# Kernel optimization log

Measured on AMD Instinct MI355X. Metric: run time of the kernel, lower is better.

The kernel has to match this reference:

```python
import jax, jax.numpy as jnp
import numpy as np

B, T, E, H, G = 8, 1024, 1024, 16, 4
D = E // H
SCALING = D ** -0.5
READER_W = 0.1  # reader_group_weight


def _heads(x):
    # [B, T, E] -> [B, H, T, D]
    return x.reshape(B, T, H, D).transpose(0, 2, 1, 3)


def setup_inputs() -> dict:
    key = jax.random.key(0)
    ks = jax.random.split(key, 16)
    s = 0.02
    return {
        "hidden_states": jax.random.normal(ks[0], (B, T, E), jnp.float32),
        "reader_token": jax.random.randint(ks[1], (B,), 0, G, dtype=jnp.int32),
        # shared (generic) projections, torch Linear convention: y = x @ W.T + b
        "Wq": jax.random.normal(ks[2], (E, E), jnp.float32) * s,
        "bq": jnp.zeros((E,), jnp.float32),
        "Wk": jax.random.normal(ks[3], (E, E), jnp.float32) * s,
        "bk": jnp.zeros((E,), jnp.float32),
        "Wv": jax.random.normal(ks[4], (E, E), jnp.float32) * s,
        "bv": jnp.zeros((E,), jnp.float32),
        "Wo": jax.random.normal(ks[5], (E, E), jnp.float32) * s,
        "bo": jnp.zeros((E,), jnp.float32),
        # stacked per-reader-group expert projections [G, E, E]
        "RWq": jax.random.normal(ks[6], (G, E, E), jnp.float32) * s,
        "Rbq": jnp.zeros((G, E), jnp.float32),
        "RWk": jax.random.normal(ks[7], (G, E, E), jnp.float32) * s,
        "Rbk": jnp.zeros((G, E), jnp.float32),
        "RWv": jax.random.normal(ks[8], (G, E, E), jnp.float32) * s,
        "Rbv": jnp.zeros((G, E), jnp.float32),
    }


def reference(hidden_states, reader_token, Wq, bq, Wk, bk, Wv, bv, Wo, bo,
              RWq, Rbq, RWk, Rbk, RWv, Rbv):
    hs = hidden_states
    # --- generic attention probs (shared weights) ---
    q = _heads((hs @ Wq.T + bq) * SCALING)          # [B,H,T,D]
    k = _heads(hs @ Wk.T + bk)                       # [B,H,T,D]
    v = _heads(hs @ Wv.T + bv)                       # [B,H,T,D]
    gen_probs = jax.nn.softmax(jnp.einsum('bhtd,bhsd->bhts', q, k), axis=-1)
    # --- reader-group attention probs (per-sample routed weights) ---
    Wq_b = RWq[reader_token]                          # [B,E,E]
    Wk_b = RWk[reader_token]
    q_r = _heads((jnp.einsum('bte,boe->bto', hs, Wq_b) + Rbq[reader_token][:, None, :]) * SCALING)
    k_r = _heads(jnp.einsum('bte,boe->bto', hs, Wk_b) + Rbk[reader_token][:, None, :])
    rdr_probs = jax.nn.softmax(jnp.einsum('bhtd,bhsd->bhts', q_r, k_r), axis=-1)
    # --- weighted combine, then attend over GENERIC value states ---
    probs = (READER_W * rdr_probs + (1.0 - READER_W) * gen_probs) / 2.0
    attn = jnp.einsum('bhts,bhsd->bhtd', probs, v)    # [B,H,T,D]
    attn = attn.transpose(0, 2, 1, 3).reshape(B, T, E)
    return attn @ Wo.T + bo
```

## Files before the change

kernel.cpp:

```cpp
#include <hip/hip_runtime.h>
#include <stdint.h>

#define AS1 __attribute__((address_space(1)))
#define AS3 __attribute__((address_space(3)))

typedef __attribute__((ext_vector_type(8))) short bf16x8;
typedef __attribute__((ext_vector_type(4))) float f32x4;

#define NB 8
#define NT 1024
#define NE 1024
#define NH 16
#define BT (NB * NT)

__device__ __forceinline__ unsigned short f2bf(float f) {
    unsigned int u = __builtin_bit_cast(unsigned int, f);
    u += 0x7FFFu + ((u >> 16) & 1u);
    return (unsigned short)(u >> 16);
}
__device__ __forceinline__ unsigned short f2bfu(float f) {
    unsigned int u = __builtin_bit_cast(unsigned int, f);
    return (unsigned short)((u + 0x8000u) >> 16);
}

__global__ void k_cvt(const float* __restrict__ in, unsigned short* __restrict__ out, int n) {
    int i = (blockIdx.x * 256 + threadIdx.x) * 4;
    if (i >= n) return;
    float4 f = *reinterpret_cast<const float4*>(in + i);
    ushort4 o;
    o.x = f2bf(f.x); o.y = f2bf(f.y); o.z = f2bf(f.z); o.w = f2bf(f.w);
    *reinterpret_cast<ushort4*>(out + i) = o;
}

struct GJob {
    const unsigned short* W;
    const float* bias;
    void* out;
    float scale;
    int routed;
};

template <bool OUT_F32>
__global__ __launch_bounds__(512, 2)
void k_gemm256(const unsigned short* __restrict__ A,
               GJob j0, GJob j1, GJob j2, GJob j3, GJob j4,
               const int* __restrict__ rt, int cpx)
{
    __shared__ __attribute__((aligned(16))) unsigned short LB[2][2][2][128 * 64];

    const int flat = blockIdx.x;
    const int wgid = (flat & 7) * cpx + (flat >> 3);
    const int pz  = wgid >> 7;
    const int rem = wgid & 127;
    const int by = rem >> 2, bx = rem & 3;
    const int m0 = by << 8, n0 = bx << 8;

    GJob jb = j0;
    if (pz == 1) jb = j1;
    else if (pz == 2) jb = j2;
    else if (pz == 3) jb = j3;
    else if (pz == 4) jb = j4;
    int g = jb.routed ? rt[m0 >> 10] : 0;
    const unsigned short* Wg = jb.W + (size_t)g * NE * NE;

    const int tid  = threadIdx.x;
    const int wid  = tid >> 6;
    const int lane = tid & 63;
    const int frow = lane & 15;
    const int g4   = lane >> 4;
    const int wm = wid >> 2, wn = wid & 3;

    const int rh0  = tid >> 3;
    const int swz8 = ((tid & 7) ^ (rh0 & 7)) * 8;
    const unsigned short* baseA = A  + (size_t)m0 * NE;
    const unsigned short* baseB = Wg + (size_t)n0 * NE;

    auto STAGE = [&](int d, int mat, int half, int kt) {
        const unsigned short* base = mat ? baseB : baseA;
#pragma unroll
        for (int j = 0; j < 2; ++j) {
            const unsigned short* src =
                base + (size_t)(half * 128 + rh0 + j * 64) * NE + kt * 64 + swz8;
            __builtin_amdgcn_global_load_lds((AS1 void*)src,
                (AS3 void*)&LB[d][mat][half][(wid * 64 + j * 512) * 8], 16, 0, 0);
        }
    };

    f32x4 acc[8][4];
#pragma unroll
    for (int m = 0; m < 8; ++m)
#pragma unroll
        for (int n = 0; n < 4; ++n) acc[m][n] = (f32x4){0.f, 0.f, 0.f, 0.f};

    bf16x8 a4[4], b4[4];
    auto RDA = [&](int d, int mh, int kh) {
#pragma unroll
        for (int mf = 0; mf < 4; ++mf) {
            int rh = mh * 64 + mf * 16 + frow;
            int off = rh * 64 + (((kh * 4 + g4) ^ (frow & 7)) * 8);
            a4[mf] = *reinterpret_cast<const bf16x8*>(&LB[d][0][wm][off]);
        }
    };
    auto RDB = [&](int d, int kh) {
#pragma unroll
        for (int nf = 0; nf < 4; ++nf) {
            int rh = (wn & 1) * 64 + nf * 16 + frow;
            int off = rh * 64 + (((kh * 4 + g4) ^ (frow & 7)) * 8);
            b4[nf] = *reinterpret_cast<const bf16x8*>(&LB[d][1][wn >> 1][off]);
        }
    };
    auto MM = [&](int mh) {
        __builtin_amdgcn_s_setprio(1);
#pragma unroll
        for (int mf = 0; mf < 4; ++mf)
#pragma unroll
            for (int nf = 0; nf < 4; ++nf)
                acc[mh * 4 + mf][nf] =
                    __builtin_amdgcn_mfma_f32_16x16x32_bf16(a4[mf], b4[nf], acc[mh * 4 + mf][nf], 0, 0, 0);
        __builtin_amdgcn_s_setprio(0);
    };

#define BARX __builtin_amdgcn_s_barrier()
#define LGK0 asm volatile("s_waitcnt lgkmcnt(0)" ::: "memory")
#define VMC2 asm volatile("s_waitcnt vmcnt(2)" ::: "memory")

    STAGE(0, 0, 0, 0); STAGE(0, 0, 1, 0); STAGE(0, 1, 0, 0); STAGE(0, 1, 1, 0);
    STAGE(1, 1, 0, 1);
    VMC2; BARX;

#pragma unroll 1
    for (int i = 0; i < 8; ++i) {
        const int t = 2 * i;
        const bool pre = (i < 7);
        RDA(0, 0, 0); RDB(0, 0); STAGE(1, 1, 1, t + 1);
        BARX; LGK0; MM(0); BARX;
        RDA(0, 1, 0); STAGE(1, 0, 0, t + 1);
        BARX; LGK0; MM(1); BARX;
        RDA(0, 0, 1); RDB(0, 1); STAGE(1, 0, 1, t + 1);
        BARX; LGK0; MM(0); BARX;
        RDA(0, 1, 1); if (pre) STAGE(0, 1, 0, t + 2);
        BARX; LGK0; MM(1); VMC2; BARX;
        RDA(1, 0, 0); RDB(1, 0); if (pre) STAGE(0, 1, 1, t + 2);
        BARX; LGK0; MM(0); BARX;
        RDA(1, 1, 0); if (pre) STAGE(0, 0, 0, t + 2);
        BARX; LGK0; MM(1); BARX;
        RDA(1, 0, 1); RDB(1, 1); if (pre) STAGE(0, 0, 1, t + 2);
        BARX; LGK0; MM(0); BARX;
        RDA(1, 1, 1); if (pre) STAGE(1, 1, 0, t + 3);
        BARX; LGK0; MM(1); VMC2; BARX;
    }
#undef BARX
#undef LGK0
#undef VMC2

    const float* biasg = jb.bias + (size_t)(jb.routed ? (rt[m0 >> 10]) : 0) * NE;
#pragma unroll
    for (int am = 0; am < 8; ++am) {
        int row = m0 + wm * 128 + am * 16 + g4 * 4;
#pragma unroll
        for (int nf = 0; nf < 4; ++nf) {
            int col = n0 + wn * 64 + nf * 16 + frow;
            float bv = biasg[col];
            f32x4 v = acc[am][nf];
#pragma unroll
            for (int r = 0; r < 4; ++r) {
                float val = (v[r] + bv) * jb.scale;
                if (OUT_F32)
                    ((float*)jb.out)[(size_t)(row + r) * NE + col] = val;
                else
                    ((unsigned short*)jb.out)[(size_t)(row + r) * NE + col] = f2bf(val);
            }
        }
    }
}

__global__ void k_vtrans(const unsigned short* __restrict__ V, unsigned short* __restrict__ Vt) {
    __shared__ unsigned short tile[64][65];
    const int blk = blockIdx.x;
    const int bh = blk >> 4;
    const int b = bh >> 4;
    const int h = bh & 15;
    const int s0 = (blk & 15) * 64;
    const int tid = threadIdx.x;
#pragma unroll
    for (int i = 0; i < 2; ++i) {
        int seg = tid + i * 256;
        int row = seg >> 3;
        int c8 = (seg & 7) * 8;
        const unsigned short* src = V + (size_t)(b * NT + s0 + row) * NE + h * 64 + c8;
        ushort4 u0 = *reinterpret_cast<const ushort4*>(src);
        ushort4 u1 = *reinterpret_cast<const ushort4*>(src + 4);
        tile[row][c8 + 0] = u0.x; tile[row][c8 + 1] = u0.y;
        tile[row][c8 + 2] = u0.z; tile[row][c8 + 3] = u0.w;
        tile[row][c8 + 4] = u1.x; tile[row][c8 + 5] = u1.y;
        tile[row][c8 + 6] = u1.z; tile[row][c8 + 7] = u1.w;
    }
    __syncthreads();
#pragma unroll
    for (int i = 0; i < 2; ++i) {
        int seg = tid + i * 256;
        int drow = seg >> 3;
        int s8 = (seg & 7) * 8;
        ushort4 u0, u1;
        u0.x = tile[s8 + 0][drow]; u0.y = tile[s8 + 1][drow];
        u0.z = tile[s8 + 2][drow]; u0.w = tile[s8 + 3][drow];
        u1.x = tile[s8 + 4][drow]; u1.y = tile[s8 + 5][drow];
        u1.z = tile[s8 + 6][drow]; u1.w = tile[s8 + 7][drow];
        unsigned short* dst = Vt + (size_t)(bh * 64 + drow) * NT + s0 + s8;
        *reinterpret_cast<ushort4*>(dst) = u0;
        *reinterpret_cast<ushort4*>(dst + 4) = u1;
    }
}

__global__ void k_attn(const unsigned short* __restrict__ Q,
                       const unsigned short* __restrict__ K,
                       const unsigned short* __restrict__ Qr,
                       const unsigned short* __restrict__ Kr,
                       const unsigned short* __restrict__ Vt,
                       unsigned short* __restrict__ attnO)
{
    constexpr int PLD = 40;
    __shared__ __attribute__((aligned(16))) unsigned short KV[2][6144];
    __shared__ __attribute__((aligned(16))) unsigned short Pg[8][16 * PLD];
    __shared__ __attribute__((aligned(16))) unsigned short Pr[8][16 * PLD];

    const int blk = (blockIdx.x & 7) * 128 + (blockIdx.x >> 3);
    const int tile = blk & 7;
    const int bh = blk >> 3;
    const int b = bh >> 4;
    const int h = bh & 15;
    const int wid = threadIdx.x >> 6;
    const int lane = threadIdx.x & 63;
    const int frow = lane & 15;
    const int g4 = lane >> 4;
    const int fk8 = g4 * 8;
    const int t0 = tile * 128 + wid * 16;

    const size_t qoff = (size_t)(b * NT + t0 + frow) * NE + h * 64;
    const bf16x8 qf0 = *reinterpret_cast<const bf16x8*>(Q + qoff + fk8);
    const bf16x8 qf1 = *reinterpret_cast<const bf16x8*>(Q + qoff + 32 + fk8);
    const bf16x8 qr0 = *reinterpret_cast<const bf16x8*>(Qr + qoff + fk8);
    const bf16x8 qr1 = *reinterpret_cast<const bf16x8*>(Qr + qoff + 32 + fk8);

    const unsigned short* Kb  = K  + (size_t)b * NT * NE + h * 64;
    const unsigned short* Krb = Kr + (size_t)b * NT * NE + h * 64;
    const unsigned short* Vtb = Vt + (size_t)bh * 64 * NT;
    unsigned short* Pgw = &Pg[wid][0];
    unsigned short* Prw = &Pr[wid][0];

    f32x4 og[4], orr[4];
    float lgp[4], lrp[4];
#pragma unroll
    for (int i = 0; i < 4; ++i) {
        og[i] = (f32x4){0.f, 0.f, 0.f, 0.f};
        orr[i] = (f32x4){0.f, 0.f, 0.f, 0.f};
        lgp[i] = 0.f; lrp[i] = 0.f;
    }

    auto stage = [&](int buf, int s0) {
#pragma unroll
        for (int i = 0; i < 2; ++i) {
            int cg = (i == 0) ? wid : (8 + wid);
            if (i == 1 && wid >= 4) break;
            int c = cg * 64 + lane;
            const unsigned short* src;
            if (cg < 8) {
                const unsigned short* base = (cg < 4) ? Kb : Krb;
                int cc = c & 255;
                int row = cc >> 3, cb = cc & 7;
                src = base + (size_t)(s0 + row) * NE + ((cb ^ (row & 7)) * 8);
            } else {
                int cc = c - 512;
                int d = cc >> 2, cb = cc & 3;
                src = Vtb + (size_t)d * NT + s0 + ((cb ^ (d & 3)) * 8);
            }
            __builtin_amdgcn_global_load_lds((AS1 void*)src, (AS3 void*)(&KV[buf][cg * 512]), 16, 0, 0);
        }
    };

    stage(0, 0);
    __syncthreads();
    int cur = 0;
    for (int t = 0; t < NT / 32; ++t) {
        if (t + 1 < NT / 32) stage(cur ^ 1, (t + 1) * 32);

        const unsigned short* Kl  = &KV[cur][0];
        const unsigned short* Krl = &KV[cur][2048];
        const unsigned short* Vl  = &KV[cur][4096];
        bf16x8 kg[2][2], kr[2][2], vb[4];
#pragma unroll
        for (int nf = 0; nf < 2; ++nf)
#pragma unroll
            for (int kh = 0; kh < 2; ++kh) {
                int idx = (nf * 16 + frow) * 64 + (((g4 + 4 * kh) ^ (frow & 7)) * 8);
                kg[nf][kh] = *reinterpret_cast<const bf16x8*>(Kl + idx);
                kr[nf][kh] = *reinterpret_cast<const bf16x8*>(Krl + idx);
            }
#pragma unroll
        for (int nf2 = 0; nf2 < 4; ++nf2)
            vb[nf2] = *reinterpret_cast<const bf16x8*>(Vl + (nf2 * 16 + frow) * 32 + ((g4 ^ (frow & 3)) * 8));

        const f32x4 z = (f32x4){0.f, 0.f, 0.f, 0.f};
        f32x4 sg0 = __builtin_amdgcn_mfma_f32_16x16x32_bf16(qf0, kg[0][0], z, 0, 0, 0);
        f32x4 sg1 = __builtin_amdgcn_mfma_f32_16x16x32_bf16(qf0, kg[1][0], z, 0, 0, 0);
        f32x4 sr0 = __builtin_amdgcn_mfma_f32_16x16x32_bf16(qr0, kr[0][0], z, 0, 0, 0);
        f32x4 sr1 = __builtin_amdgcn_mfma_f32_16x16x32_bf16(qr0, kr[1][0], z, 0, 0, 0);
        sg0 = __builtin_amdgcn_mfma_f32_16x16x32_bf16(qf1, kg[0][1], sg0, 0, 0, 0);
        sg1 = __builtin_amdgcn_mfma_f32_16x16x32_bf16(qf1, kg[1][1], sg1, 0, 0, 0);
        sr0 = __builtin_amdgcn_mfma_f32_16x16x32_bf16(qr1, kr[0][1], sr0, 0, 0, 0);
        sr1 = __builtin_amdgcn_mfma_f32_16x16x32_bf16(qr1, kr[1][1], sr1, 0, 0, 0);

#pragma unroll
        for (int r = 0; r < 4; ++r) {
            float pg0 = __expf(sg0[r]);
            float pg1 = __expf(sg1[r]);
            float pr0 = __expf(sr0[r]);
            float pr1 = __expf(sr1[r]);
            lgp[r] += pg0 + pg1;
            lrp[r] += pr0 + pr1;
            const int row = (g4 * 4 + r) * PLD;
            Pgw[row + frow]      = f2bfu(pg0);
            Pgw[row + 16 + frow] = f2bfu(pg1);
            Prw[row + frow]      = f2bfu(pr0);
            Prw[row + 16 + frow] = f2bfu(pr1);
        }
        asm volatile("s_waitcnt lgkmcnt(0)" ::: "memory");
        bf16x8 pag = *reinterpret_cast<const bf16x8*>(Pgw + frow * PLD + fk8);
        bf16x8 par = *reinterpret_cast<const bf16x8*>(Prw + frow * PLD + fk8);
        og[0]  = __builtin_amdgcn_mfma_f32_16x16x32_bf16(pag, vb[0], og[0], 0, 0, 0);
        orr[0] = __builtin_amdgcn_mfma_f32_16x16x32_bf16(par, vb[0], orr[0], 0, 0, 0);
        og[1]  = __builtin_amdgcn_mfma_f32_16x16x32_bf16(pag, vb[1], og[1], 0, 0, 0);
        orr[1] = __builtin_amdgcn_mfma_f32_16x16x32_bf16(par, vb[1], orr[1], 0, 0, 0);
        og[2]  = __builtin_amdgcn_mfma_f32_16x16x32_bf16(pag, vb[2], og[2], 0, 0, 0);
        orr[2] = __builtin_amdgcn_mfma_f32_16x16x32_bf16(par, vb[2], orr[2], 0, 0, 0);
        og[3]  = __builtin_amdgcn_mfma_f32_16x16x32_bf16(pag, vb[3], og[3], 0, 0, 0);
        orr[3] = __builtin_amdgcn_mfma_f32_16x16x32_bf16(par, vb[3], orr[3], 0, 0, 0);

        __syncthreads();
        cur ^= 1;
    }

#pragma unroll
    for (int off = 1; off <= 8; off <<= 1) {
#pragma unroll
        for (int r = 0; r < 4; ++r) {
            lgp[r] += __shfl_xor(lgp[r], off);
            lrp[r] += __shfl_xor(lrp[r], off);
        }
    }
    float ig[4], ir[4];
#pragma unroll
    for (int r = 0; r < 4; ++r) { ig[r] = 0.45f / lgp[r]; ir[r] = 0.05f / lrp[r]; }
#pragma unroll
    for (int nf2 = 0; nf2 < 4; ++nf2) {
#pragma unroll
        for (int r = 0; r < 4; ++r) {
            float val = og[nf2][r] * ig[r] + orr[nf2][r] * ir[r];
            int t = t0 + g4 * 4 + r;
            attnO[(size_t)(b * NT + t) * NE + h * 64 + nf2 * 16 + frow] = f2bf(val);
        }
    }
}

extern "C" void kernel_launch(void* const* d_in, const int* in_sizes, int n_in,
                              void* d_out, int out_size, void* d_ws, size_t ws_size,
                              hipStream_t stream)
{
    const float* hs  = (const float*)d_in[0];
    const int*   rt  = (const int*)d_in[1];
    const float* Wq  = (const float*)d_in[2];
    const float* bq  = (const float*)d_in[3];
    const float* Wk  = (const float*)d_in[4];
    const float* bk  = (const float*)d_in[5];
    const float* Wv  = (const float*)d_in[6];
    const float* bv  = (const float*)d_in[7];
    const float* Wo  = (const float*)d_in[8];
    const float* bo  = (const float*)d_in[9];
    const float* RWq = (const float*)d_in[10];
    const float* Rbq = (const float*)d_in[11];
    const float* RWk = (const float*)d_in[12];
    const float* Rbk = (const float*)d_in[13];

    unsigned short* w = (unsigned short*)d_ws;
    const size_t NBT = (size_t)BT * NE;
    const size_t NW  = (size_t)NE * NE;
    unsigned short* hsB  = w; w += NBT;
    unsigned short* Qb   = w; w += NBT;
    unsigned short* Kb   = w; w += NBT;
    unsigned short* Vb   = w; w += NBT;
    unsigned short* Qrb  = w; w += NBT;
    unsigned short* Krb  = w; w += NBT;
    unsigned short* Vtb  = w; w += NBT;
    unsigned short* atb  = w; w += NBT;
    unsigned short* WqB  = w; w += NW;
    unsigned short* WkB  = w; w += NW;
    unsigned short* WvB  = w; w += NW;
    unsigned short* WoB  = w; w += NW;
    unsigned short* RWqB = w; w += 4 * NW;
    unsigned short* RWkB = w; w += 4 * NW;

    k_cvt<<<dim3((unsigned)(NBT / 1024)), dim3(256), 0, stream>>>(hs, hsB, (int)NBT);
    k_cvt<<<dim3((unsigned)(NW / 1024)), dim3(256), 0, stream>>>(Wq, WqB, (int)NW);
    k_cvt<<<dim3((unsigned)(NW / 1024)), dim3(256), 0, stream>>>(Wk, WkB, (int)NW);
    k_cvt<<<dim3((unsigned)(NW / 1024)), dim3(256), 0, stream>>>(Wv, WvB, (int)NW);
    k_cvt<<<dim3((unsigned)(NW / 1024)), dim3(256), 0, stream>>>(Wo, WoB, (int)NW);
    k_cvt<<<dim3((unsigned)(4 * NW / 1024)), dim3(256), 0, stream>>>(RWq, RWqB, (int)(4 * NW));
    k_cvt<<<dim3((unsigned)(4 * NW / 1024)), dim3(256), 0, stream>>>(RWk, RWkB, (int)(4 * NW));

    GJob jq  = { WqB,  bq,  Qb,  0.125f, 0 };
    GJob jk  = { WkB,  bk,  Kb,  1.0f,   0 };
    GJob jv  = { WvB,  bv,  Vb,  1.0f,   0 };
    GJob jrq = { RWqB, Rbq, Qrb, 0.125f, 1 };
    GJob jrk = { RWkB, Rbk, Krb, 1.0f,   1 };
    k_gemm256<false><<<dim3(640), dim3(512), 0, stream>>>(hsB, jq, jk, jv, jrq, jrk, rt, 80);

    k_vtrans<<<dim3(NB * NH * 16), dim3(256), 0, stream>>>(Vb, Vtb);
    k_attn<<<dim3(NB * NH * 8), dim3(512), 0, stream>>>(Qb, Kb, Qrb, Krb, Vtb, atb);

    GJob jo = { WoB, bo, d_out, 1.0f, 0 };
    k_gemm256<true><<<dim3(128), dim3(512), 0, stream>>>(atb, jo, jo, jo, jo, jo, nullptr, 16);
}
```

Measured before the change: 274.7 us.

## Restructure attention loop to 64-key tiles and merge conversion kernels

The attention kernel now stages 64 keys per iteration (K, Kr and transposed V each as 64x64 tiles), halving the number of barrier-synchronised iterations. It computes S with K as the A operand so each lane holds a row's probabilities, packs them with v_cvt_pk_bf16 and writes them to a single shared P buffer that is reused for the generic and reader passes. Row sums collapse to one scalar per lane. The seven fp32-to-bf16 conversion launches are merged into one kernel to cut launch overhead. Shared memory per block grows, which may limit occupancy despite the launch_bounds hint, and the conversion kernel still spends most of its work converting weights on every call.

```diff
diff --git a/kernel.cpp b/kernel.cpp
--- a/kernel.cpp
+++ b/kernel.cpp
@@ -18,18 +18,34 @@
     u += 0x7FFFu + ((u >> 16) & 1u);
     return (unsigned short)(u >> 16);
 }
-__device__ __forceinline__ unsigned short f2bfu(float f) {
-    unsigned int u = __builtin_bit_cast(unsigned int, f);
-    return (unsigned short)((u + 0x8000u) >> 16);
-}
-
-__global__ void k_cvt(const float* __restrict__ in, unsigned short* __restrict__ out, int n) {
-    int i = (blockIdx.x * 256 + threadIdx.x) * 4;
-    if (i >= n) return;
-    float4 f = *reinterpret_cast<const float4*>(in + i);
+__device__ __forceinline__ unsigned int cvt_pk_bf16(float lo, float hi) {
+    unsigned int r;
+    asm("v_cvt_pk_bf16_f32 %0, %1, %2" : "=v"(r) : "v"(lo), "v"(hi));
+    return r;
+}
+
+__global__ void k_cvt7(const float* __restrict__ hs, unsigned short* __restrict__ hsB,
+                       const float* __restrict__ w1, unsigned short* __restrict__ w1B,
+                       const float* __restrict__ w2, unsigned short* __restrict__ w2B,
+                       const float* __restrict__ w3, unsigned short* __restrict__ w3B,
+                       const float* __restrict__ w4, unsigned short* __restrict__ w4B,
+                       const float* __restrict__ r1, unsigned short* __restrict__ r1B,
+                       const float* __restrict__ r2, unsigned short* __restrict__ r2B)
+{
+    int blk = blockIdx.x;
+    const float* s; unsigned short* d; int base;
+    if      (blk < 8192)  { s = hs; d = hsB; base = 0; }
+    else if (blk < 9216)  { s = w1; d = w1B; base = 8192; }
+    else if (blk < 10240) { s = w2; d = w2B; base = 9216; }
+    else if (blk < 11264) { s = w3; d = w3B; base = 10240; }
+    else if (blk < 12288) { s = w4; d = w4B; base = 11264; }
+    else if (blk < 16384) { s = r1; d = r1B; base = 12288; }
+    else                  { s = r2; d = r2B; base = 16384; }
+    int i = ((blk - base) * 256 + threadIdx.x) * 4;
+    float4 f = *reinterpret_cast<const float4*>(s + i);
     ushort4 o;
     o.x = f2bf(f.x); o.y = f2bf(f.y); o.z = f2bf(f.z); o.w = f2bf(f.w);
-    *reinterpret_cast<ushort4*>(out + i) = o;
+    *reinterpret_cast<ushort4*>(d + i) = o;
 }
 
 struct GJob {
@@ -212,17 +228,17 @@
     }
 }
 
-__global__ void k_attn(const unsigned short* __restrict__ Q,
-                       const unsigned short* __restrict__ K,
-                       const unsigned short* __restrict__ Qr,
-                       const unsigned short* __restrict__ Kr,
-                       const unsigned short* __restrict__ Vt,
-                       unsigned short* __restrict__ attnO)
+__global__ __launch_bounds__(512, 4)
+void k_attn(const unsigned short* __restrict__ Q,
+            const unsigned short* __restrict__ K,
+            const unsigned short* __restrict__ Qr,
+            const unsigned short* __restrict__ Kr,
+            const unsigned short* __restrict__ Vt,
+            unsigned short* __restrict__ attnO)
 {
-    constexpr int PLD = 40;
-    __shared__ __attribute__((aligned(16))) unsigned short KV[2][6144];
-    __shared__ __attribute__((aligned(16))) unsigned short Pg[8][16 * PLD];
-    __shared__ __attribute__((aligned(16))) unsigned short Pr[8][16 * PLD];
+    constexpr int PLD = 72;
+    __shared__ __attribute__((aligned(16))) unsigned short KV[2][3 * 4096];
+    __shared__ __attribute__((aligned(16))) unsigned short Ps[8][16 * PLD];
 
     const int blk = (blockIdx.x & 7) * 128 + (blockIdx.x >> 3);
     const int tile = blk & 7;
@@ -233,6 +249,7 @@
     const int lane = threadIdx.x & 63;
     const int frow = lane & 15;
     const int g4 = lane >> 4;
+    const int f7 = frow & 7;
     const int fk8 = g4 * 8;
     const int t0 = tile * 128 + wid * 16;
 
@@ -245,119 +262,121 @@
     const unsigned short* Kb  = K  + (size_t)b * NT * NE + h * 64;
     const unsigned short* Krb = Kr + (size_t)b * NT * NE + h * 64;
     const unsigned short* Vtb = Vt + (size_t)bh * 64 * NT;
-    unsigned short* Pgw = &Pg[wid][0];
-    unsigned short* Prw = &Pr[wid][0];
+    unsigned short* Pw = &Ps[wid][0];
+    unsigned short* Prow = Pw + frow * PLD;
 
     f32x4 og[4], orr[4];
-    float lgp[4], lrp[4];
+    float lgp = 0.f, lrp = 0.f;
 #pragma unroll
     for (int i = 0; i < 4; ++i) {
         og[i] = (f32x4){0.f, 0.f, 0.f, 0.f};
         orr[i] = (f32x4){0.f, 0.f, 0.f, 0.f};
-        lgp[i] = 0.f; lrp[i] = 0.f;
-    }
-
+    }
+
+    const int srow = threadIdx.x >> 3;
+    const int scb8 = ((threadIdx.x & 7) ^ (srow & 7)) * 8;
     auto stage = [&](int buf, int s0) {
-#pragma unroll
-        for (int i = 0; i < 2; ++i) {
-            int cg = (i == 0) ? wid : (8 + wid);
-            if (i == 1 && wid >= 4) break;
-            int c = cg * 64 + lane;
-            const unsigned short* src;
-            if (cg < 8) {
-                const unsigned short* base = (cg < 4) ? Kb : Krb;
-                int cc = c & 255;
-                int row = cc >> 3, cb = cc & 7;
-                src = base + (size_t)(s0 + row) * NE + ((cb ^ (row & 7)) * 8);
-            } else {
-                int cc = c - 512;
-                int d = cc >> 2, cb = cc & 3;
-                src = Vtb + (size_t)d * NT + s0 + ((cb ^ (d & 3)) * 8);
-            }
-            __builtin_amdgcn_global_load_lds((AS1 void*)src, (AS3 void*)(&KV[buf][cg * 512]), 16, 0, 0);
-        }
+        const unsigned short* sK = Kb  + (size_t)(s0 + srow) * NE + scb8;
+        const unsigned short* sR = Krb + (size_t)(s0 + srow) * NE + scb8;
+        const unsigned short* sV = Vtb + (size_t)srow * NT + s0 + scb8;
+        __builtin_amdgcn_global_load_lds((AS1 void*)sK, (AS3 void*)(&KV[buf][wid * 512]), 16, 0, 0);
+        __builtin_amdgcn_global_load_lds((AS1 void*)sR, (AS3 void*)(&KV[buf][4096 + wid * 512]), 16, 0, 0);
+        __builtin_amdgcn_global_load_lds((AS1 void*)sV, (AS3 void*)(&KV[buf][8192 + wid * 512]), 16, 0, 0);
     };
 
     stage(0, 0);
     __syncthreads();
     int cur = 0;
-    for (int t = 0; t < NT / 32; ++t) {
-        if (t + 1 < NT / 32) stage(cur ^ 1, (t + 1) * 32);
-
+    const f32x4 z = (f32x4){0.f, 0.f, 0.f, 0.f};
+#pragma unroll 1
+    for (int t = 0; t < NT / 64; ++t) {
+        if (t < NT / 64 - 1) stage(cur ^ 1, (t + 1) * 64);
         const unsigned short* Kl  = &KV[cur][0];
-        const unsigned short* Krl = &KV[cur][2048];
-        const unsigned short* Vl  = &KV[cur][4096];
-        bf16x8 kg[2][2], kr[2][2], vb[4];
-#pragma unroll
-        for (int nf = 0; nf < 2; ++nf)
-#pragma unroll
-            for (int kh = 0; kh < 2; ++kh) {
-                int idx = (nf * 16 + frow) * 64 + (((g4 + 4 * kh) ^ (frow & 7)) * 8);
-                kg[nf][kh] = *reinterpret_cast<const bf16x8*>(Kl + idx);
-                kr[nf][kh] = *reinterpret_cast<const bf16x8*>(Krl + idx);
+        const unsigned short* Krl = &KV[cur][4096];
+        const unsigned short* Vl  = &KV[cur][8192];
+
+        f32x4 sg[4], sr[4];
+#pragma unroll
+        for (int nf = 0; nf < 4; ++nf) {
+            const int ro = (nf * 16 + frow) * 64;
+            bf16x8 kA = *reinterpret_cast<const bf16x8*>(Kl + ro + ((g4 ^ f7) * 8));
+            bf16x8 kB = *reinterpret_cast<const bf16x8*>(Kl + ro + (((4 + g4) ^ f7) * 8));
+            bf16x8 rA = *reinterpret_cast<const bf16x8*>(Krl + ro + ((g4 ^ f7) * 8));
+            bf16x8 rB = *reinterpret_cast<const bf16x8*>(Krl + ro + (((4 + g4) ^ f7) * 8));
+            sg[nf] = __builtin_amdgcn_mfma_f32_16x16x32_bf16(kA, qf0, z, 0, 0, 0);
+            sg[nf] = __builtin_amdgcn_mfma_f32_16x16x32_bf16(kB, qf1, sg[nf], 0, 0, 0);
+            sr[nf] = __builtin_amdgcn_mfma_f32_16x16x32_bf16(rA, qr0, z, 0, 0, 0);
+            sr[nf] = __builtin_amdgcn_mfma_f32_16x16x32_bf16(rB, qr1, sr[nf], 0, 0, 0);
+        }
+
+#pragma unroll
+        for (int nf = 0; nf < 4; ++nf) {
+            float p0 = __expf(sg[nf][0]), p1 = __expf(sg[nf][1]);
+            float p2 = __expf(sg[nf][2]), p3 = __expf(sg[nf][3]);
+            lgp += (p0 + p1) + (p2 + p3);
+            uint2 wv;
+            wv.x = cvt_pk_bf16(p0, p1);
+            wv.y = cvt_pk_bf16(p2, p3);
+            *reinterpret_cast<uint2*>(Prow + nf * 16 + g4 * 4) = wv;
+        }
+        asm volatile("s_waitcnt lgkmcnt(0)" ::: "memory");
+        {
+            bf16x8 pa0 = *reinterpret_cast<const bf16x8*>(Prow + fk8);
+            bf16x8 pa1 = *reinterpret_cast<const bf16x8*>(Prow + 32 + fk8);
+#pragma unroll
+            for (int nf2 = 0; nf2 < 4; ++nf2) {
+                const int vo = (nf2 * 16 + frow) * 64;
+                bf16x8 v0 = *reinterpret_cast<const bf16x8*>(Vl + vo + ((g4 ^ f7) * 8));
+                bf16x8 v1 = *reinterpret_cast<const bf16x8*>(Vl + vo + (((4 + g4) ^ f7) * 8));
+                og[nf2] = __builtin_amdgcn_mfma_f32_16x16x32_bf16(pa0, v0, og[nf2], 0, 0, 0);
+                og[nf2] = __builtin_amdgcn_mfma_f32_16x16x32_bf16(pa1, v1, og[nf2], 0, 0, 0);
             }
-#pragma unroll
-        for (int nf2 = 0; nf2 < 4; ++nf2)
-            vb[nf2] = *reinterpret_cast<const bf16x8*>(Vl + (nf2 * 16 + frow) * 32 + ((g4 ^ (frow & 3)) * 8));
-
-        const f32x4 z = (f32x4){0.f, 0.f, 0.f, 0.f};
-        f32x4 sg0 = __builtin_amdgcn_mfma_f32_16x16x32_bf16(qf0, kg[0][0], z, 0, 0, 0);
-        f32x4 sg1 = __builtin_amdgcn_mfma_f32_16x16x32_bf16(qf0, kg[1][0], z, 0, 0, 0);
-        f32x4 sr0 = __builtin_amdgcn_mfma_f32_16x16x32_bf16(qr0, kr[0][0], z, 0, 0, 0);
-        f32x4 sr1 = __builtin_amdgcn_mfma_f32_16x16x32_bf16(qr0, kr[1][0], z, 0, 0, 0);
-        sg0 = __builtin_amdgcn_mfma_f32_16x16x32_bf16(qf1, kg[0][1], sg0, 0, 0, 0);
-        sg1 = __builtin_amdgcn_mfma_f32_16x16x32_bf16(qf1, kg[1][1], sg1, 0, 0, 0);
-        sr0 = __builtin_amdgcn_mfma_f32_16x16x32_bf16(qr1, kr[0][1], sr0, 0, 0, 0);
-        sr1 = __builtin_amdgcn_mfma_f32_16x16x32_bf16(qr1, kr[1][1], sr1, 0, 0, 0);
-
-#pragma unroll
-        for (int r = 0; r < 4; ++r) {
-            float pg0 = __expf(sg0[r]);
-            float pg1 = __expf(sg1[r]);
-            float pr0 = __expf(sr0[r]);
-            float pr1 = __expf(sr1[r]);
-            lgp[r] += pg0 + pg1;
-            lrp[r] += pr0 + pr1;
-            const int row = (g4 * 4 + r) * PLD;
-            Pgw[row + frow]      = f2bfu(pg0);
-            Pgw[row + 16 + frow] = f2bfu(pg1);
-            Prw[row + frow]      = f2bfu(pr0);
-            Prw[row + 16 + frow] = f2bfu(pr1);
+        }
+
+#pragma unroll
+        for (int nf = 0; nf < 4; ++nf) {
+            float p0 = __expf(sr[nf][0]), p1 = __expf(sr[nf][1]);
+            float p2 = __expf(sr[nf][2]), p3 = __expf(sr[nf][3]);
+            lrp += (p0 + p1) + (p2 + p3);
+            uint2 wv;
+            wv.x = cvt_pk_bf16(p0, p1);
+            wv.y = cvt_pk_bf16(p2, p3);
+            *reinterpret_cast<uint2*>(Prow + nf * 16 + g4 * 4) = wv;
         }
         asm volatile("s_waitcnt lgkmcnt(0)" ::: "memory");
-        bf16x8 pag = *reinterpret_cast<const bf16x8*>(Pgw + frow * PLD + fk8);
-        bf16x8 par = *reinterpret_cast<const bf16x8*>(Prw + frow * PLD + fk8);
-        og[0]  = __builtin_amdgcn_mfma_f32_16x16x32_bf16(pag, vb[0], og[0], 0, 0, 0);
-        orr[0] = __builtin_amdgcn_mfma_f32_16x16x32_bf16(par, vb[0], orr[0], 0, 0, 0);
-        og[1]  = __builtin_amdgcn_mfma_f32_16x16x32_bf16(pag, vb[1], og[1], 0, 0, 0);
-        orr[1] = __builtin_amdgcn_mfma_f32_16x16x32_bf16(par, vb[1], orr[1], 0, 0, 0);
-        og[2]  = __builtin_amdgcn_mfma_f32_16x16x32_bf16(pag, vb[2], og[2], 0, 0, 0);
-        orr[2] = __builtin_amdgcn_mfma_f32_16x16x32_bf16(par, vb[2], orr[2], 0, 0, 0);
-        og[3]  = __builtin_amdgcn_mfma_f32_16x16x32_bf16(pag, vb[3], og[3], 0, 0, 0);
-        orr[3] = __builtin_amdgcn_mfma_f32_16x16x32_bf16(par, vb[3], orr[3], 0, 0, 0);
+        {
+            bf16x8 pa0 = *reinterpret_cast<const bf16x8*>(Prow + fk8);
+            bf16x8 pa1 = *reinterpret_cast<const bf16x8*>(Prow + 32 + fk8);
+#pragma unroll
+            for (int nf2 = 0; nf2 < 4; ++nf2) {
+                const int vo = (nf2 * 16 + frow) * 64;
+                bf16x8 v0 = *reinterpret_cast<const bf16x8*>(Vl + vo + ((g4 ^ f7) * 8));
+                bf16x8 v1 = *reinterpret_cast<const bf16x8*>(Vl + vo + (((4 + g4) ^ f7) * 8));
+                orr[nf2] = __builtin_amdgcn_mfma_f32_16x16x32_bf16(pa0, v0, orr[nf2], 0, 0, 0);
+                orr[nf2] = __builtin_amdgcn_mfma_f32_16x16x32_bf16(pa1, v1, orr[nf2], 0, 0, 0);
+            }
+        }
 
         __syncthreads();
         cur ^= 1;
     }
 
-#pragma unroll
-    for (int off = 1; off <= 8; off <<= 1) {
+    lgp += __shfl_xor(lgp, 16); lgp += __shfl_xor(lgp, 32);
+    lrp += __shfl_xor(lrp, 16); lrp += __shfl_xor(lrp, 32);
+    float ig = 0.45f / lgp, ir = 0.05f / lrp;
+    float igr[4], irr[4];
+#pragma unroll
+    for (int r = 0; r < 4; ++r) {
+        igr[r] = __shfl(ig, g4 * 4 + r);
+        irr[r] = __shfl(ir, g4 * 4 + r);
+    }
+#pragma unroll
+    for (int nf2 = 0; nf2 < 4; ++nf2) {
 #pragma unroll
         for (int r = 0; r < 4; ++r) {
-            lgp[r] += __shfl_xor(lgp[r], off);
-            lrp[r] += __shfl_xor(lrp[r], off);
-        }
-    }
-    float ig[4], ir[4];
-#pragma unroll
-    for (int r = 0; r < 4; ++r) { ig[r] = 0.45f / lgp[r]; ir[r] = 0.05f / lrp[r]; }
-#pragma unroll
-    for (int nf2 = 0; nf2 < 4; ++nf2) {
-#pragma unroll
-        for (int r = 0; r < 4; ++r) {
-            float val = og[nf2][r] * ig[r] + orr[nf2][r] * ir[r];
-            int t = t0 + g4 * 4 + r;
-            attnO[(size_t)(b * NT + t) * NE + h * 64 + nf2 * 16 + frow] = f2bf(val);
+            float val = og[nf2][r] * igr[r] + orr[nf2][r] * irr[r];
+            int tq = t0 + g4 * 4 + r;
+            attnO[(size_t)(b * NT + tq) * NE + h * 64 + nf2 * 16 + frow] = f2bf(val);
         }
     }
 }
@@ -399,13 +418,8 @@
     unsigned short* RWqB = w; w += 4 * NW;
     unsigned short* RWkB = w; w += 4 * NW;
 
-    k_cvt<<<dim3((unsigned)(NBT / 1024)), dim3(256), 0, stream>>>(hs, hsB, (int)NBT);
-    k_cvt<<<dim3((unsigned)(NW / 1024)), dim3(256), 0, stream>>>(Wq, WqB, (int)NW);
-    k_cvt<<<dim3((unsigned)(NW / 1024)), dim3(256), 0, stream>>>(Wk, WkB, (int)NW);
-    k_cvt<<<dim3((unsigned)(NW / 1024)), dim3(256), 0, stream>>>(Wv, WvB, (int)NW);
-    k_cvt<<<dim3((unsigned)(NW / 1024)), dim3(256), 0, stream>>>(Wo, WoB, (int)NW);
-    k_cvt<<<dim3((unsigned)(4 * NW / 1024)), dim3(256), 0, stream>>>(RWq, RWqB, (int)(4 * NW));
-    k_cvt<<<dim3((unsigned)(4 * NW / 1024)), dim3(256), 0, stream>>>(RWk, RWkB, (int)(4 * NW));
+    k_cvt7<<<dim3(20480), dim3(256), 0, stream>>>(hs, hsB, Wq, WqB, Wk, WkB, Wv, WvB,
+                                                  Wo, WoB, RWq, RWqB, RWk, RWkB);
 
     GJob jq  = { WqB,  bq,  Qb,  0.125f, 0 };
     GJob jk  = { WkB,  bk,  Kb,  1.0f,   0 };
```

Result: faster. 262.5 us (-4.4%).
